# Performance work log

Measured on AMD Instinct MI355X. Metric: run time of the kernel, lower is better.

## Reference

```python
import math
import jax, jax.numpy as jnp
import numpy as np

D_MODEL = 1024
N_HEADS = 16
D_K = D_MODEL // N_HEADS


def _alibi_slopes(n_heads):
    # Faithful to the torch _get_slopes: slopes[i] = 2**(-8 + i), subsampled if
    # n_heads is not a power of two.
    power = 2 ** math.ceil(math.log2(n_heads))
    slopes = np.array([2.0 ** (-8 + i) for i in range(power)], dtype=np.float32)
    if n_heads != power:
        ratio = power // n_heads
        slopes = slopes[np.arange(0, power, ratio)][:n_heads]
    return jnp.asarray(slopes)


def setup_inputs() -> dict:
    key = jax.random.key(0)
    ks = jax.random.split(key, 11)
    B, S, D = 2, 2048, D_MODEL
    w = 0.02  # weight init scale
    return {
        "query": jax.random.normal(ks[0], (B, S, D), jnp.float32),
        "key": jax.random.normal(ks[1], (B, S, D), jnp.float32),
        "value": jax.random.normal(ks[2], (B, S, D), jnp.float32),
        "Wq": jax.random.normal(ks[3], (D, D), jnp.float32) * w,
        "bq": jax.random.normal(ks[4], (D,), jnp.float32) * w,
        "Wk": jax.random.normal(ks[5], (D, D), jnp.float32) * w,
        "bk": jax.random.normal(ks[6], (D,), jnp.float32) * w,
        "Wv": jax.random.normal(ks[7], (D, D), jnp.float32) * w,
        "bv": jax.random.normal(ks[8], (D,), jnp.float32) * w,
        "Wo": jax.random.normal(ks[9], (D, D), jnp.float32) * w,
        "bo": jax.random.normal(ks[10], (D,), jnp.float32) * w,
    }


def reference(query, key, value, Wq, bq, Wk, bk, Wv, bv, Wo, bo):
    B, Sq, D = query.shape
    Sk = key.shape[1]
    H, dk = N_HEADS, D_K

    # projections (torch Linear: x @ W.T + b)
    q = (query @ Wq.T + bq).reshape(B, Sq, H, dk).transpose(0, 2, 1, 3)  # [B,H,Sq,dk]
    k = (key @ Wk.T + bk).reshape(B, Sk, H, dk).transpose(0, 2, 1, 3)    # [B,H,Sk,dk]
    v = (value @ Wv.T + bv).reshape(B, Sk, H, dk).transpose(0, 2, 1, 3)  # [B,H,Sk,dk]

    scores = jnp.einsum("bhqd,bhkd->bhqk", q, k) / jnp.sqrt(jnp.float32(dk))

    # ALiBi bias: slopes[h] * (i - j), non-causal path (is_causal=False)
    dist = (jnp.arange(Sq)[:, None] - jnp.arange(Sk)[None, :]).astype(scores.dtype)
    slopes = _alibi_slopes(H)
    scores = scores + slopes[None, :, None, None] * dist[None, None, :, :]

    attn = jax.nn.softmax(scores, axis=-1)
    out = jnp.einsum("bhqk,bhkd->bhqd", attn, v)          # [B,H,Sq,dk]
    out = out.transpose(0, 2, 1, 3).reshape(B, Sq, D)     # [B,Sq,D]
    return out @ Wo.T + bo
```

## Files before the change

kernel.cpp:

```cpp
#include <hip/hip_runtime.h>

typedef __bf16 bf16_t;
typedef bf16_t bf16x8 __attribute__((ext_vector_type(8)));
typedef float f32x4 __attribute__((ext_vector_type(4)));
typedef float f32x16 __attribute__((ext_vector_type(16)));
typedef unsigned short u16x4 __attribute__((ext_vector_type(4)));
typedef unsigned int u32x4v __attribute__((ext_vector_type(4)));
typedef unsigned int u32;

#define DEV static __device__ __forceinline__


DEV unsigned short f2bf(float f) {
  unsigned int u = __builtin_bit_cast(unsigned int, f);
  u = (u + 0x7fffu + ((u >> 16) & 1u)) >> 16;
  return (unsigned short)u;
}

DEV float fexp2(float x) {
  float r;
  asm("v_exp_f32 %0, %1" : "=v"(r) : "v"(x));
  return r;
}

DEV u32 cvtpk(float lo, float hi_) {
  u32 r;
  asm("v_cvt_pk_bf16_f32 %0, %1, %2" : "=v"(r) : "v"(lo), "v"(hi_));
  return r;
}

DEV void plswap(u32& a, u32& b) {
  asm("v_permlane32_swap_b32 %0, %1" : "+v"(a), "+v"(b));
}

DEV void async_ld16(const unsigned short* gsrc, unsigned short* lbase, int lane) {
#if __has_builtin(__builtin_amdgcn_global_load_lds)
  __builtin_amdgcn_global_load_lds(
      (const __attribute__((address_space(1))) unsigned int*)(const void*)gsrc,
      (__attribute__((address_space(3))) unsigned int*)(void*)lbase, 16, 0, 0);
#else
  *reinterpret_cast<u32x4v*>(reinterpret_cast<char*>(lbase) + lane * 16) =
      *reinterpret_cast<const u32x4v*>(gsrc);
#endif
}


DEV void cvt_body(const float* __restrict__ src, unsigned short* __restrict__ dst, int i) {
  const float4* s = reinterpret_cast<const float4*>(src) + (size_t)i * 2;
  float4 a = s[0], c = s[1];
  u16x4 lo = {f2bf(a.x), f2bf(a.y), f2bf(a.z), f2bf(a.w)};
  u16x4 hi = {f2bf(c.x), f2bf(c.y), f2bf(c.z), f2bf(c.w)};
  u16x4* d = reinterpret_cast<u16x4*>(dst) + (size_t)i * 2;
  d[0] = lo;
  d[1] = hi;
}

__global__ __launch_bounds__(256) void cvt_all(
    const float* __restrict__ q, const float* __restrict__ k, const float* __restrict__ v,
    const float* __restrict__ Wq, const float* __restrict__ Wk, const float* __restrict__ Wv,
    const float* __restrict__ Wo, unsigned short* dq, unsigned short* dk, unsigned short* dv,
    unsigned short* dWq, unsigned short* dWk, unsigned short* dWv, unsigned short* dWo) {
  const int bid = blockIdx.x;
  const float* src;
  unsigned short* dst;
  int i;
  if (bid < 6144) {
    const int z = bid >> 11;
    src = z == 0 ? q : z == 1 ? k : v;
    dst = z == 0 ? dq : z == 1 ? dk : dv;
    i = (bid & 2047) * 256 + threadIdx.x;
  } else {
    const int z = (bid - 6144) >> 9;
    src = z == 0 ? Wq : z == 1 ? Wk : z == 2 ? Wv : Wo;
    dst = z == 0 ? dWq : z == 1 ? dWk : z == 2 ? dWv : dWo;
    i = ((bid - 6144) & 511) * 256 + threadIdx.x;
  }
  cvt_body(src, dst, i);
}


DEV void stage_b128(const unsigned short* __restrict__ G, int row0, int k0,
                    unsigned short* lbuf, int lane, int wv) {
#pragma unroll
  for (int r = 0; r < 4; ++r) {
    const int rowB = (r * 4 + wv) * 8 + (lane >> 3);
    const int chunk = (lane & 7) ^ (rowB & 7);
    async_ld16(G + (size_t)(row0 + rowB) * 1024 + k0 + chunk * 8, lbuf + (r * 4 + wv) * 512,
               lane);
  }
}

DEV void mfma_step(const unsigned short* lA, const unsigned short* lB, int lane, int wm, int wn,
                   f32x4 acc[4][4]) {
#pragma unroll
  for (int kk = 0; kk < 2; ++kk) {
    bf16x8 af[4], bfr[4];
#pragma unroll
    for (int f = 0; f < 4; ++f) {
      const int rowA = wm * 64 + f * 16 + (lane & 15);
      const int cA = (kk * 4 + (lane >> 4)) ^ (rowA & 7);
      af[f] = *reinterpret_cast<const bf16x8*>(lA + rowA * 64 + cA * 8);
      const int rowB = wn * 64 + f * 16 + (lane & 15);
      const int cB = (kk * 4 + (lane >> 4)) ^ (rowB & 7);
      bfr[f] = *reinterpret_cast<const bf16x8*>(lB + rowB * 64 + cB * 8);
    }
#pragma unroll
    for (int i = 0; i < 4; ++i)
#pragma unroll
      for (int j = 0; j < 4; ++j)
        acc[i][j] = __builtin_amdgcn_mfma_f32_16x16x32_bf16(af[i], bfr[j], acc[i][j], 0, 0, 0);
  }
}

DEV void gemm_core(const unsigned short* __restrict__ X, const unsigned short* __restrict__ W,
                   unsigned short* lA0, unsigned short* lA1, unsigned short* lB0,
                   unsigned short* lB1, int bm0, int bn0, int lane, int wv, int wm, int wn,
                   f32x4 acc[4][4]) {
  stage_b128(X, bm0, 0, lA0, lane, wv);
  stage_b128(W, bn0, 0, lB0, lane, wv);
  __syncthreads();
  for (int kt = 0; kt < 16; ++kt) {
    unsigned short* lA = (kt & 1) ? lA1 : lA0;
    unsigned short* lB = (kt & 1) ? lB1 : lB0;
    unsigned short* nA = (kt & 1) ? lA0 : lA1;
    unsigned short* nB = (kt & 1) ? lB0 : lB1;
    if (kt < 15) {
      stage_b128(X, bm0, (kt + 1) * 64, nA, lane, wv);
      stage_b128(W, bn0, (kt + 1) * 64, nB, lane, wv);
    }
    mfma_step(lA, lB, lane, wm, wn, acc);
    __syncthreads();
  }
}


__global__ __launch_bounds__(256) void gemm_qkv_kernel(
    const unsigned short* __restrict__ Xq, const unsigned short* __restrict__ Xk,
    const unsigned short* __restrict__ Xv, const unsigned short* __restrict__ Wq,
    const unsigned short* __restrict__ Wk, const unsigned short* __restrict__ Wv,
    const float* __restrict__ bq, const float* __restrict__ bk, const float* __restrict__ bv,
    unsigned short* __restrict__ Qp, unsigned short* __restrict__ Kp,
    unsigned short* __restrict__ Vp, unsigned* __restrict__ nb2) {
  __shared__ unsigned short lA[2][8192];
  __shared__ unsigned short lB[2][8192];
  const unsigned short* X;
  const unsigned short* W;
  const float* bias;
  unsigned short* dst;
  if (blockIdx.z == 0) { X = Xq; W = Wq; bias = bq; dst = Qp; }
  else if (blockIdx.z == 1) { X = Xk; W = Wk; bias = bk; dst = Kp; }
  else { X = Xv; W = Wv; bias = bv; dst = Vp; }
  const bool zV = (blockIdx.z == 2);
  const bool zK = (blockIdx.z == 1) && (nb2 != nullptr);
  const int lane = threadIdx.x & 63, wv = threadIdx.x >> 6;
  const int wm = wv >> 1, wn = wv & 1;
  const int bm0 = blockIdx.x * 128, bn0 = blockIdx.y * 128;
  f32x4 acc[4][4] = {};
  gemm_core(X, W, lA[0], lA[1], lB[0], lB[1], bm0, bn0, lane, wv, wm, wn, acc);
  float rowmax = 0.0f;
#pragma unroll
  for (int i = 0; i < 4; ++i) {
    const int mbase = bm0 + wm * 64 + i * 16 + ((lane >> 4) << 2);
#pragma unroll
    for (int r = 0; r < 4; ++r) {
      const int m = mbase + r;
      const int b = m >> 11, s = m & 2047;
      float ssp = 0.0f;
#pragma unroll
      for (int j = 0; j < 4; ++j) {
        const int n = bn0 + wn * 64 + j * 16 + (lane & 15);
        const float val = acc[i][j][r] + bias[n];
        const unsigned short v16 = f2bf(val);
        const int h = n >> 6, d = n & 63;
        if (zV)
          dst[((size_t)(b * 16 + h) * 64 + d) * 2048 + s] = v16;
        else
          dst[((size_t)(b * 16 + h) * 2048 + s) * 64 + d] = v16;
        ssp = __builtin_fmaf(val, val, ssp);
      }
      if (zK) {
        ssp += __shfl_xor(ssp, 1);
        ssp += __shfl_xor(ssp, 2);
        ssp += __shfl_xor(ssp, 4);
        ssp += __shfl_xor(ssp, 8);
        rowmax = fmaxf(rowmax, ssp);
      }
    }
  }
  if (zK) {
    rowmax = fmaxf(rowmax, __shfl_xor(rowmax, 16));
    rowmax = fmaxf(rowmax, __shfl_xor(rowmax, 32));
    if (lane == 0) {
      const int bh = (bm0 >> 11) * 16 + blockIdx.y * 2 + wn;
      atomicMax(nb2 + bh, __float_as_uint(rowmax));
    }
  }
}


__global__ __launch_bounds__(256) void gemm_out_kernel(const unsigned short* __restrict__ X,
                                                       const unsigned short* __restrict__ W,
                                                       const float* __restrict__ bias,
                                                       float* __restrict__ out) {
  __shared__ unsigned short lA[2][8192];
  __shared__ unsigned short lB[2][8192];
  const int lane = threadIdx.x & 63, wv = threadIdx.x >> 6;
  const int wm = wv >> 1, wn = wv & 1;
  const int bm0 = blockIdx.x * 128, bn0 = blockIdx.y * 128;
  f32x4 acc[4][4] = {};
  gemm_core(X, W, lA[0], lA[1], lB[0], lB[1], bm0, bn0, lane, wv, wm, wn, acc);
#pragma unroll
  for (int i = 0; i < 4; ++i) {
    const int mbase = bm0 + wm * 64 + i * 16 + ((lane >> 4) << 2);
#pragma unroll
    for (int j = 0; j < 4; ++j) {
      const int n = bn0 + wn * 64 + j * 16 + (lane & 15);
      const float bia = bias[n];
#pragma unroll
      for (int r = 0; r < 4; ++r) out[(size_t)(mbase + r) * 1024 + n] = acc[i][j][r] + bia;
    }
  }
}


__global__ __launch_bounds__(256) void knorm_kernel(const unsigned short* __restrict__ Kp,
                                                    unsigned* __restrict__ nb2) {
  const int bh = blockIdx.y;
  const int s = blockIdx.x * 256 + threadIdx.x;
  const u32x4v* row = reinterpret_cast<const u32x4v*>(Kp + ((size_t)bh * 2048 + s) * 64);
  float ss = 0.0f;
#pragma unroll
  for (int c = 0; c < 8; ++c) {
    u32x4v u = row[c];
#pragma unroll
    for (int e = 0; e < 4; ++e) {
      const float lo = __builtin_bit_cast(float, u[e] << 16);
      const float hi = __builtin_bit_cast(float, u[e] & 0xFFFF0000u);
      ss = __builtin_fmaf(lo, lo, ss);
      ss = __builtin_fmaf(hi, hi, ss);
    }
  }
#pragma unroll
  for (int off = 1; off <= 32; off <<= 1) ss = fmaxf(ss, __shfl_xor(ss, off));
  if ((threadIdx.x & 63) == 0) atomicMax(nb2 + bh, __float_as_uint(ss));
}


__global__ __launch_bounds__(128) void attn_prepass(const unsigned short* __restrict__ Qp,
                                                    const unsigned short* __restrict__ Kp,
                                                    const unsigned* __restrict__ nb2,
                                                    float* __restrict__ mfA,
                                                    float* __restrict__ bltA) {
  __shared__ float sred[4];
  const int lane = threadIdx.x & 63, wv = threadIdx.x >> 6;
  const int lq = lane & 31, hi = lane >> 5;
  const int qt = blockIdx.x, bh = blockIdx.y, h = bh & 15;
  const float L2E = 1.4426950408889634f;
  const float slope2 = ldexpf(L2E, h - 8);
  const float SC2 = 0.125f * L2E;
  const size_t headoff = (size_t)bh * 2048 * 64;
  const unsigned short* Qh = Qp + headoff;
  const unsigned short* Kh = Kp + headoff;
  const int q_glob = qt * 64 + wv * 32 + lq;

  bf16x8 qf[4];
#pragma unroll
  for (int tt = 0; tt < 4; ++tt)
    qf[tt] = *reinterpret_cast<const bf16x8*>(Qh + (size_t)q_glob * 64 + tt * 16 + hi * 8);

  float qq = 0.0f;
#pragma unroll
  for (int tt = 0; tt < 4; ++tt)
#pragma unroll
    for (int e = 0; e < 8; ++e) {
      const float x = (float)qf[tt][e];
      qq = __builtin_fmaf(x, x, qq);
    }
  qq += __shfl_xor(qq, 32);
#pragma unroll
  for (int off = 1; off <= 16; off <<= 1) qq = fmaxf(qq, __shfl_xor(qq, off));

  f32x16 s0 = {}, s1 = {};
#pragma unroll
  for (int tt = 0; tt < 4; ++tt) {
    bf16x8 k0 = *reinterpret_cast<const bf16x8*>(Kh + (size_t)lq * 64 + tt * 16 + hi * 8);
    s0 = __builtin_amdgcn_mfma_f32_32x32x16_bf16(k0, qf[tt], s0, 0, 0, 0);
    bf16x8 k1 = *reinterpret_cast<const bf16x8*>(Kh + (size_t)(32 + lq) * 64 + tt * 16 + hi * 8);
    s1 = __builtin_amdgcn_mfma_f32_32x32x16_bf16(k1, qf[tt], s1, 0, 0, 0);
  }
  float zmax = -3.0e38f;
#pragma unroll
  for (int r = 0; r < 16; ++r) {
    const float cb = -slope2 * (float)(4 * hi + (r & 3) + 8 * (r >> 2));
    const float x0 = __builtin_fmaf(s0[r], SC2, cb);
    const float x1 = __builtin_fmaf(s1[r], SC2, cb - slope2 * 32.0f);
    zmax = fmaxf(zmax, fmaxf(x0, x1));
  }
  zmax = fmaxf(zmax, __shfl_xor(zmax, 32));
  float zmin = zmax;
#pragma unroll
  for (int off = 1; off <= 16; off <<= 1) zmin = fminf(zmin, __shfl_xor(zmin, off));
  if (lane == 0) {
    sred[wv] = zmin;
    sred[2 + wv] = qq;
  }
  __syncthreads();
  if (threadIdx.x == 0) {
    const float mf = fminf(sred[0], sred[1]);
    const float qn = sqrtf(fmaxf(sred[2], sred[3]));
    const float nk = sqrtf(__uint_as_float(nb2[bh]));
    mfA[bh * 32 + qt] = mf;
    bltA[bh * 32 + qt] = qn * nk * SC2;
  }
}


DEV void stage_tile64(const unsigned short* __restrict__ Gbase, size_t stride, int colbase,
                      unsigned short* lbuf, int lane, int wv) {
#pragma unroll
  for (int i = 0; i < 4; ++i) {
    const int r = i * 16 + wv * 8 + (lane >> 3);
    const int chunk = (lane & 7) ^ (r & 7);
    async_ld16(Gbase + (size_t)r * stride + colbase + chunk * 8, lbuf + (i * 16 + wv * 8) * 64,
               lane);
  }
}

__global__ __launch_bounds__(128) void attn_split_kernel(
    const unsigned short* __restrict__ Qp, const unsigned short* __restrict__ Kp,
    const unsigned short* __restrict__ VTp, const float* __restrict__ mfA,
    const float* __restrict__ bltA, float* __restrict__ ML, float* __restrict__ Opart, int Ct,
    int nsplit) {
  __shared__ unsigned short Kb[2][64 * 64];
  __shared__ unsigned short Vb[2][64 * 64];
  const int lane = threadIdx.x & 63, wv = threadIdx.x >> 6;
  const int lq = lane & 31, hi = lane >> 5;
  const int qt = blockIdx.x, sp = blockIdx.y, bh = blockIdx.z;
  const int h = bh & 15;
  const int idx = bh * 32 + qt;
  const float L2E = 1.4426950408889634f;
  const float slope2 = ldexpf(L2E, h - 8);
  const float SC2 = 0.125f * L2E;
  const float m_floor = mfA[idx], blt = bltA[idx];
  const float tf = (blt - m_floor + 34.0f) / (slope2 * 64.0f);
  const int T_act = min(32, (int)tf + 1);
  const int t0 = sp * Ct;
  const int nt = min(Ct, T_act - t0);
  float* mlb = ML + ((size_t)idx * nsplit + sp) * 128;
  if (nt <= 0) {
    mlb[threadIdx.x] = threadIdx.x < 64 ? -3.0e38f : 0.0f;
    return;
  }
  float* ob = Opart + ((size_t)idx * nsplit + sp) * 4096;
  const size_t headoff = (size_t)bh * 2048 * 64;
  const unsigned short* Qh = Qp + headoff;
  const unsigned short* Kh = Kp + headoff;
  const unsigned short* VTh = VTp + headoff;
  const int q_glob = qt * 64 + wv * 32 + lq;

  float cb0[16], cb1[16];
#pragma unroll
  for (int r = 0; r < 16; ++r) {
    cb0[r] = -slope2 * (float)(4 * hi + (r & 3) + 8 * (r >> 2));
    cb1[r] = cb0[r] - slope2 * 32.0f;
  }

  bf16x8 qf[4];
#pragma unroll
  for (int tt = 0; tt < 4; ++tt)
    qf[tt] = *reinterpret_cast<const bf16x8*>(Qh + (size_t)q_glob * 64 + tt * 16 + hi * 8);

  stage_tile64(Kh + (size_t)(t0 * 64) * 64, 64, 0, Kb[0], lane, wv);
  stage_tile64(VTh, 2048, t0 * 64, Vb[0], lane, wv);
  __syncthreads();

  f32x16 acc0 = {}, acc1 = {};
  float m_run = m_floor, l_run = 0.0f;

  for (int ti = 0; ti < nt; ++ti) {
    const int kv0 = (t0 + ti) * 64;
    const float s2k = slope2 * (float)kv0;
    const unsigned short* Kc = Kb[ti & 1];
    const unsigned short* Vc = Vb[ti & 1];
    if (ti + 1 < nt) {
      stage_tile64(Kh + (size_t)(kv0 + 64) * 64, 64, 0, Kb[(ti + 1) & 1], lane, wv);
      stage_tile64(VTh, 2048, kv0 + 64, Vb[(ti + 1) & 1], lane, wv);
    }
    f32x16 s0 = {}, s1 = {};
    __builtin_amdgcn_s_setprio(1);
#pragma unroll
    for (int tt = 0; tt < 4; ++tt) {
      {
        const int row = lq;
        const int ch = (tt * 2 + hi) ^ (row & 7);
        bf16x8 kf = *reinterpret_cast<const bf16x8*>(Kc + row * 64 + ch * 8);
        s0 = __builtin_amdgcn_mfma_f32_32x32x16_bf16(kf, qf[tt], s0, 0, 0, 0);
      }
      {
        const int row = 32 + lq;
        const int ch = (tt * 2 + hi) ^ (row & 7);
        bf16x8 kf = *reinterpret_cast<const bf16x8*>(Kc + row * 64 + ch * 8);
        s1 = __builtin_amdgcn_mfma_f32_32x32x16_bf16(kf, qf[tt], s1, 0, 0, 0);
      }
    }
    __builtin_amdgcn_s_setprio(0);
    float zmax = -3.0e38f;
#pragma unroll
    for (int r = 0; r < 16; ++r) {
      s0[r] = __builtin_fmaf(s0[r], SC2, cb0[r]);
      s1[r] = __builtin_fmaf(s1[r], SC2, cb1[r]);
      zmax = fmaxf(zmax, fmaxf(s0[r], s1[r]));
    }
    zmax = fmaxf(zmax, __shfl_xor(zmax, 32));
    const float tmax_true = zmax - s2k;
    if (__any(tmax_true > m_run + 8.0f)) {
      const float m_new = fmaxf(m_run, tmax_true);
      const float alpha = fexp2(m_run - m_new);
      m_run = m_new;
      l_run *= alpha;
      acc0 *= alpha;
      acc1 *= alpha;
    }
    const float mm = m_run + s2k;
    float ps0 = 0.0f, ps1 = 0.0f;
#pragma unroll
    for (int r = 0; r < 16; ++r) {
      const float p0 = fexp2(s0[r] - mm);
      const float p1 = fexp2(s1[r] - mm);
      s0[r] = p0;
      s1[r] = p1;
      ps0 += p0;
      ps1 += p1;
    }
    float psum = ps0 + ps1;
    psum += __shfl_xor(psum, 32);
    l_run += psum;
    bf16x8 pf[4];
#pragma unroll
    for (int half = 0; half < 2; ++half) {
      u32 w0 = cvtpk(s0[half * 8 + 0], s0[half * 8 + 1]);
      u32 w2 = cvtpk(s0[half * 8 + 4], s0[half * 8 + 5]);
      plswap(w0, w2);
      u32 w1 = cvtpk(s0[half * 8 + 2], s0[half * 8 + 3]);
      u32 w3 = cvtpk(s0[half * 8 + 6], s0[half * 8 + 7]);
      plswap(w1, w3);
      u32x4v ww = {w0, w1, w2, w3};
      pf[half] = __builtin_bit_cast(bf16x8, ww);
    }
#pragma unroll
    for (int half = 0; half < 2; ++half) {
      u32 w0 = cvtpk(s1[half * 8 + 0], s1[half * 8 + 1]);
      u32 w2 = cvtpk(s1[half * 8 + 4], s1[half * 8 + 5]);
      plswap(w0, w2);
      u32 w1 = cvtpk(s1[half * 8 + 2], s1[half * 8 + 3]);
      u32 w3 = cvtpk(s1[half * 8 + 6], s1[half * 8 + 7]);
      plswap(w1, w3);
      u32x4v ww = {w0, w1, w2, w3};
      pf[2 + half] = __builtin_bit_cast(bf16x8, ww);
    }
    __builtin_amdgcn_s_setprio(1);
#pragma unroll
    for (int tt = 0; tt < 4; ++tt) {
      {
        const int row = lq;
        const int ch = (tt * 2 + hi) ^ (row & 7);
        bf16x8 vf = *reinterpret_cast<const bf16x8*>(Vc + row * 64 + ch * 8);
        acc0 = __builtin_amdgcn_mfma_f32_32x32x16_bf16(vf, pf[tt], acc0, 0, 0, 0);
      }
      {
        const int row = 32 + lq;
        const int ch = (tt * 2 + hi) ^ (row & 7);
        bf16x8 vf = *reinterpret_cast<const bf16x8*>(Vc + row * 64 + ch * 8);
        acc1 = __builtin_amdgcn_mfma_f32_32x32x16_bf16(vf, pf[tt], acc1, 0, 0, 0);
      }
    }
    __builtin_amdgcn_s_setprio(0);
    __syncthreads();
  }
  const int qloc = wv * 32 + lq;
  if (hi == 0) {
    mlb[qloc] = m_run;
    mlb[64 + qloc] = l_run;
  }
#pragma unroll
  for (int g = 0; g < 4; ++g) {
    f32x4 w0, w1;
#pragma unroll
    for (int e = 0; e < 4; ++e) {
      w0[e] = acc0[g * 4 + e];
      w1[e] = acc1[g * 4 + e];
    }
    *reinterpret_cast<f32x4*>(ob + qloc * 64 + g * 8 + 4 * hi) = w0;
    *reinterpret_cast<f32x4*>(ob + qloc * 64 + 32 + g * 8 + 4 * hi) = w1;
  }
}


__global__ __launch_bounds__(256) void attn_combine(const float* __restrict__ ML,
                                                    const float* __restrict__ Opart,
                                                    unsigned short* __restrict__ Ob, int nsplit) {
  const int idx = blockIdx.x;
  const int bh = idx >> 5, qt = idx & 31;
  const int h = bh & 15, b = bh >> 4;
  const int q = threadIdx.x >> 2, d0 = (threadIdx.x & 3) * 16;
  const float* mlb = ML + (size_t)idx * nsplit * 128;
  const float* ob = Opart + (size_t)idx * nsplit * 4096;
  float m_g = -3.0e38f;
  for (int s = 0; s < nsplit; ++s) m_g = fmaxf(m_g, mlb[s * 128 + q]);
  float l = 0.0f;
  f32x4 acc[4] = {};
  for (int s = 0; s < nsplit; ++s) {
    const float ms = mlb[s * 128 + q], ls = mlb[s * 128 + 64 + q];
    const float w = fexp2(ms - m_g);
    const float wl = w * ls;
    if (wl > 0.0f) {
      l += wl;
      const f32x4* src = reinterpret_cast<const f32x4*>(ob + (size_t)s * 4096 + q * 64 + d0);
#pragma unroll
      for (int j = 0; j < 4; ++j) {
        f32x4 v = src[j];
#pragma unroll
        for (int e = 0; e < 4; ++e) acc[j][e] = __builtin_fmaf(w, v[e], acc[j][e]);
      }
    }
  }
  const float invl = 1.0f / l;
  unsigned short* orow = Ob + ((size_t)(b * 2048 + qt * 64 + q)) * 1024 + h * 64 + d0;
#pragma unroll
  for (int j = 0; j < 4; ++j) {
    u16x4 pk;
#pragma unroll
    for (int e = 0; e < 4; ++e) pk[e] = f2bf(acc[j][e] * invl);
    *reinterpret_cast<u16x4*>(orow + j * 4) = pk;
  }
}


extern "C" void kernel_launch(void* const* d_in, const int* in_sizes, int n_in, void* d_out,
                              int out_size, void* d_ws, size_t ws_size, hipStream_t stream) {
  const float* q = (const float*)d_in[0];
  const float* k = (const float*)d_in[1];
  const float* v = (const float*)d_in[2];
  const float* Wq = (const float*)d_in[3];
  const float* bq = (const float*)d_in[4];
  const float* Wk = (const float*)d_in[5];
  const float* bk = (const float*)d_in[6];
  const float* Wv = (const float*)d_in[7];
  const float* bv = (const float*)d_in[8];
  const float* Wo = (const float*)d_in[9];
  const float* bo = (const float*)d_in[10];

  char* ws = (char*)d_ws;
  const size_t MB = 1024 * 1024;
  unsigned short* qb = (unsigned short*)(ws + 0 * MB);
  unsigned short* kb = (unsigned short*)(ws + 8 * MB);
  unsigned short* vb = (unsigned short*)(ws + 16 * MB);
  unsigned short* Wqb = (unsigned short*)(ws + 24 * MB);
  unsigned short* Wkb = (unsigned short*)(ws + 26 * MB);
  unsigned short* Wvb = (unsigned short*)(ws + 28 * MB);
  unsigned short* Wob = (unsigned short*)(ws + 30 * MB);
  unsigned short* Qp = (unsigned short*)(ws + 32 * MB);
  unsigned short* Kp = (unsigned short*)(ws + 40 * MB);
  unsigned short* VTp = (unsigned short*)(ws + 48 * MB);
  unsigned short* Obf = (unsigned short*)(ws + 0 * MB);

  int nsplit;
  float *mfA, *bltA, *ML, *Opart;
  unsigned* nb2;
  bool fold_knorm;
  if (ws_size >= (size_t)121 * MB) nsplit = 4;
  else if (ws_size >= (size_t)89 * MB) nsplit = 2;
  else nsplit = 1;
  if (ws_size >= (size_t)73 * MB) {
    fold_knorm = true;
    nb2 = (unsigned*)(ws + 56 * MB);
    mfA = (float*)(ws + 24 * MB + 4096);
    bltA = (float*)(ws + 24 * MB + 8192);
    ML = (float*)(ws + 26 * MB + 65536);
    Opart = (float*)(ws + 56 * MB + 4096);
  } else {
    fold_knorm = false;
    nsplit = 1;
    nb2 = (unsigned*)(ws + 26 * MB);
    mfA = (float*)(ws + 26 * MB + 4096);
    bltA = (float*)(ws + 26 * MB + 8192);
    ML = (float*)(ws + 26 * MB + 65536);
    Opart = (float*)(ws + 8 * MB);
  }
  const int Ct = 32 / nsplit;

  cvt_all<<<8192, 256, 0, stream>>>(q, k, v, Wq, Wk, Wv, Wo, qb, kb, vb, Wqb, Wkb, Wvb, Wob);
  hipMemsetAsync(nb2, 0, 64 * sizeof(unsigned), stream);
  gemm_qkv_kernel<<<dim3(32, 8, 3), 256, 0, stream>>>(qb, kb, vb, Wqb, Wkb, Wvb, bq, bk, bv, Qp,
                                                      Kp, VTp, fold_knorm ? nb2 : nullptr);
  if (!fold_knorm) knorm_kernel<<<dim3(8, 32), 256, 0, stream>>>(Kp, nb2);
  attn_prepass<<<dim3(32, 32), 128, 0, stream>>>(Qp, Kp, nb2, mfA, bltA);
  attn_split_kernel<<<dim3(32, nsplit, 32), 128, 0, stream>>>(Qp, Kp, VTp, mfA, bltA, ML, Opart,
                                                              Ct, nsplit);
  attn_combine<<<1024, 256, 0, stream>>>(ML, Opart, Obf, nsplit);
  gemm_out_kernel<<<dim3(32, 8), 256, 0, stream>>>(Obf, Wob, bo, (float*)d_out);
}
```

Measured before the change: 124.6 us.

## Fuse attention prepass into split kernel and fold nb2 zeroing into convert

Removes the separate attn_prepass launch. Each attn_split block now computes its own query-norm and first-tile score minimum, from which it derives the skip bound. The nb2 memset is moved into the cvt_all kernel when fold_knorm holds, and the GEMM staging precomputes per-row global pointers and fully unrolls the k-loop. This saves two launches and a round-trip through mfA/bltA, but every split block (nsplit of them per q-tile) redoes the prepass work, and the unrolled loop adds code size and register pressure.

```diff
diff --git a/kernel.cpp b/kernel.cpp
--- a/kernel.cpp
+++ b/kernel.cpp
@@ -59,8 +59,10 @@
     const float* __restrict__ q, const float* __restrict__ k, const float* __restrict__ v,
     const float* __restrict__ Wq, const float* __restrict__ Wk, const float* __restrict__ Wv,
     const float* __restrict__ Wo, unsigned short* dq, unsigned short* dk, unsigned short* dv,
-    unsigned short* dWq, unsigned short* dWk, unsigned short* dWv, unsigned short* dWo) {
+    unsigned short* dWq, unsigned short* dWk, unsigned short* dWv, unsigned short* dWo,
+    unsigned* __restrict__ nb2z) {
   const int bid = blockIdx.x;
+  if (nb2z != nullptr && bid == 0 && threadIdx.x < 64) nb2z[threadIdx.x] = 0u;
   const float* src;
   unsigned short* dst;
   int i;
@@ -79,17 +81,6 @@
 }
 
 
-DEV void stage_b128(const unsigned short* __restrict__ G, int row0, int k0,
-                    unsigned short* lbuf, int lane, int wv) {
-#pragma unroll
-  for (int r = 0; r < 4; ++r) {
-    const int rowB = (r * 4 + wv) * 8 + (lane >> 3);
-    const int chunk = (lane & 7) ^ (rowB & 7);
-    async_ld16(G + (size_t)(row0 + rowB) * 1024 + k0 + chunk * 8, lbuf + (r * 4 + wv) * 512,
-               lane);
-  }
-}
-
 DEV void mfma_step(const unsigned short* lA, const unsigned short* lB, int lane, int wm, int wn,
                    f32x4 acc[4][4]) {
 #pragma unroll
@@ -116,17 +107,33 @@
                    unsigned short* lA0, unsigned short* lA1, unsigned short* lB0,
                    unsigned short* lB1, int bm0, int bn0, int lane, int wv, int wm, int wn,
                    f32x4 acc[4][4]) {
-  stage_b128(X, bm0, 0, lA0, lane, wv);
-  stage_b128(W, bn0, 0, lB0, lane, wv);
+  const unsigned short* pa[4];
+  const unsigned short* pb[4];
+#pragma unroll
+  for (int r = 0; r < 4; ++r) {
+    const int row = (r * 4 + wv) * 8 + (lane >> 3);
+    const int chunk = (lane & 7) ^ (row & 7);
+    pa[r] = X + (size_t)(bm0 + row) * 1024 + chunk * 8;
+    pb[r] = W + (size_t)(bn0 + row) * 1024 + chunk * 8;
+  }
+#pragma unroll
+  for (int r = 0; r < 4; ++r) {
+    async_ld16(pa[r], lA0 + (r * 4 + wv) * 512, lane);
+    async_ld16(pb[r], lB0 + (r * 4 + wv) * 512, lane);
+  }
   __syncthreads();
+#pragma unroll
   for (int kt = 0; kt < 16; ++kt) {
-    unsigned short* lA = (kt & 1) ? lA1 : lA0;
-    unsigned short* lB = (kt & 1) ? lB1 : lB0;
+    const unsigned short* lA = (kt & 1) ? lA1 : lA0;
+    const unsigned short* lB = (kt & 1) ? lB1 : lB0;
     unsigned short* nA = (kt & 1) ? lA0 : lA1;
     unsigned short* nB = (kt & 1) ? lB0 : lB1;
     if (kt < 15) {
-      stage_b128(X, bm0, (kt + 1) * 64, nA, lane, wv);
-      stage_b128(W, bn0, (kt + 1) * 64, nB, lane, wv);
+#pragma unroll
+      for (int r = 0; r < 4; ++r) {
+        async_ld16(pa[r] + (kt + 1) * 64, nA + (r * 4 + wv) * 512, lane);
+        async_ld16(pb[r] + (kt + 1) * 64, nB + (r * 4 + wv) * 512, lane);
+      }
     }
     mfma_step(lA, lB, lane, wm, wn, acc);
     __syncthreads();
@@ -246,75 +253,6 @@
 }
 
 
-__global__ __launch_bounds__(128) void attn_prepass(const unsigned short* __restrict__ Qp,
-                                                    const unsigned short* __restrict__ Kp,
-                                                    const unsigned* __restrict__ nb2,
-                                                    float* __restrict__ mfA,
-                                                    float* __restrict__ bltA) {
-  __shared__ float sred[4];
-  const int lane = threadIdx.x & 63, wv = threadIdx.x >> 6;
-  const int lq = lane & 31, hi = lane >> 5;
-  const int qt = blockIdx.x, bh = blockIdx.y, h = bh & 15;
-  const float L2E = 1.4426950408889634f;
-  const float slope2 = ldexpf(L2E, h - 8);
-  const float SC2 = 0.125f * L2E;
-  const size_t headoff = (size_t)bh * 2048 * 64;
-  const unsigned short* Qh = Qp + headoff;
-  const unsigned short* Kh = Kp + headoff;
-  const int q_glob = qt * 64 + wv * 32 + lq;
-
-  bf16x8 qf[4];
-#pragma unroll
-  for (int tt = 0; tt < 4; ++tt)
-    qf[tt] = *reinterpret_cast<const bf16x8*>(Qh + (size_t)q_glob * 64 + tt * 16 + hi * 8);
-
-  float qq = 0.0f;
-#pragma unroll
-  for (int tt = 0; tt < 4; ++tt)
-#pragma unroll
-    for (int e = 0; e < 8; ++e) {
-      const float x = (float)qf[tt][e];
-      qq = __builtin_fmaf(x, x, qq);
-    }
-  qq += __shfl_xor(qq, 32);
-#pragma unroll
-  for (int off = 1; off <= 16; off <<= 1) qq = fmaxf(qq, __shfl_xor(qq, off));
-
-  f32x16 s0 = {}, s1 = {};
-#pragma unroll
-  for (int tt = 0; tt < 4; ++tt) {
-    bf16x8 k0 = *reinterpret_cast<const bf16x8*>(Kh + (size_t)lq * 64 + tt * 16 + hi * 8);
-    s0 = __builtin_amdgcn_mfma_f32_32x32x16_bf16(k0, qf[tt], s0, 0, 0, 0);
-    bf16x8 k1 = *reinterpret_cast<const bf16x8*>(Kh + (size_t)(32 + lq) * 64 + tt * 16 + hi * 8);
-    s1 = __builtin_amdgcn_mfma_f32_32x32x16_bf16(k1, qf[tt], s1, 0, 0, 0);
-  }
-  float zmax = -3.0e38f;
-#pragma unroll
-  for (int r = 0; r < 16; ++r) {
-    const float cb = -slope2 * (float)(4 * hi + (r & 3) + 8 * (r >> 2));
-    const float x0 = __builtin_fmaf(s0[r], SC2, cb);
-    const float x1 = __builtin_fmaf(s1[r], SC2, cb - slope2 * 32.0f);
-    zmax = fmaxf(zmax, fmaxf(x0, x1));
-  }
-  zmax = fmaxf(zmax, __shfl_xor(zmax, 32));
-  float zmin = zmax;
-#pragma unroll
-  for (int off = 1; off <= 16; off <<= 1) zmin = fminf(zmin, __shfl_xor(zmin, off));
-  if (lane == 0) {
-    sred[wv] = zmin;
-    sred[2 + wv] = qq;
-  }
-  __syncthreads();
-  if (threadIdx.x == 0) {
-    const float mf = fminf(sred[0], sred[1]);
-    const float qn = sqrtf(fmaxf(sred[2], sred[3]));
-    const float nk = sqrtf(__uint_as_float(nb2[bh]));
-    mfA[bh * 32 + qt] = mf;
-    bltA[bh * 32 + qt] = qn * nk * SC2;
-  }
-}
-
-
 DEV void stage_tile64(const unsigned short* __restrict__ Gbase, size_t stride, int colbase,
                       unsigned short* lbuf, int lane, int wv) {
 #pragma unroll
@@ -328,11 +266,11 @@
 
 __global__ __launch_bounds__(128) void attn_split_kernel(
     const unsigned short* __restrict__ Qp, const unsigned short* __restrict__ Kp,
-    const unsigned short* __restrict__ VTp, const float* __restrict__ mfA,
-    const float* __restrict__ bltA, float* __restrict__ ML, float* __restrict__ Opart, int Ct,
-    int nsplit) {
+    const unsigned short* __restrict__ VTp, const unsigned* __restrict__ nb2,
+    float* __restrict__ ML, float* __restrict__ Opart, int Ct, int nsplit) {
   __shared__ unsigned short Kb[2][64 * 64];
   __shared__ unsigned short Vb[2][64 * 64];
+  __shared__ float sred[4];
   const int lane = threadIdx.x & 63, wv = threadIdx.x >> 6;
   const int lq = lane & 31, hi = lane >> 5;
   const int qt = blockIdx.x, sp = blockIdx.y, bh = blockIdx.z;
@@ -341,17 +279,8 @@
   const float L2E = 1.4426950408889634f;
   const float slope2 = ldexpf(L2E, h - 8);
   const float SC2 = 0.125f * L2E;
-  const float m_floor = mfA[idx], blt = bltA[idx];
-  const float tf = (blt - m_floor + 34.0f) / (slope2 * 64.0f);
-  const int T_act = min(32, (int)tf + 1);
   const int t0 = sp * Ct;
-  const int nt = min(Ct, T_act - t0);
   float* mlb = ML + ((size_t)idx * nsplit + sp) * 128;
-  if (nt <= 0) {
-    mlb[threadIdx.x] = threadIdx.x < 64 ? -3.0e38f : 0.0f;
-    return;
-  }
-  float* ob = Opart + ((size_t)idx * nsplit + sp) * 4096;
   const size_t headoff = (size_t)bh * 2048 * 64;
   const unsigned short* Qh = Qp + headoff;
   const unsigned short* Kh = Kp + headoff;
@@ -372,7 +301,56 @@
 
   stage_tile64(Kh + (size_t)(t0 * 64) * 64, 64, 0, Kb[0], lane, wv);
   stage_tile64(VTh, 2048, t0 * 64, Vb[0], lane, wv);
+
+  float qq = 0.0f;
+#pragma unroll
+  for (int tt = 0; tt < 4; ++tt)
+#pragma unroll
+    for (int e = 0; e < 8; ++e) {
+      const float x = (float)qf[tt][e];
+      qq = __builtin_fmaf(x, x, qq);
+    }
+  qq += __shfl_xor(qq, 32);
+#pragma unroll
+  for (int off = 1; off <= 16; off <<= 1) qq = fmaxf(qq, __shfl_xor(qq, off));
+  {
+    f32x16 s0 = {}, s1 = {};
+#pragma unroll
+    for (int tt = 0; tt < 4; ++tt) {
+      bf16x8 k0 = *reinterpret_cast<const bf16x8*>(Kh + (size_t)lq * 64 + tt * 16 + hi * 8);
+      s0 = __builtin_amdgcn_mfma_f32_32x32x16_bf16(k0, qf[tt], s0, 0, 0, 0);
+      bf16x8 k1 =
+          *reinterpret_cast<const bf16x8*>(Kh + (size_t)(32 + lq) * 64 + tt * 16 + hi * 8);
+      s1 = __builtin_amdgcn_mfma_f32_32x32x16_bf16(k1, qf[tt], s1, 0, 0, 0);
+    }
+    float zmax = -3.0e38f;
+#pragma unroll
+    for (int r = 0; r < 16; ++r) {
+      const float x0 = __builtin_fmaf(s0[r], SC2, cb0[r]);
+      const float x1 = __builtin_fmaf(s1[r], SC2, cb1[r]);
+      zmax = fmaxf(zmax, fmaxf(x0, x1));
+    }
+    zmax = fmaxf(zmax, __shfl_xor(zmax, 32));
+    float zmin = zmax;
+#pragma unroll
+    for (int off = 1; off <= 16; off <<= 1) zmin = fminf(zmin, __shfl_xor(zmin, off));
+    if (lane == 0) {
+      sred[wv] = zmin;
+      sred[2 + wv] = qq;
+    }
+  }
   __syncthreads();
+  const float m_floor = fminf(sred[0], sred[1]);
+  const float qn = sqrtf(fmaxf(sred[2], sred[3]));
+  const float blt = qn * sqrtf(__uint_as_float(nb2[bh])) * SC2;
+  const float tf = (blt - m_floor + 34.0f) / (slope2 * 64.0f);
+  const int T_act = min(32, (int)tf + 1);
+  const int nt = min(Ct, T_act - t0);
+  if (nt <= 0) {
+    mlb[threadIdx.x] = threadIdx.x < 64 ? -3.0e38f : 0.0f;
+    return;
+  }
+  float* ob = Opart + ((size_t)idx * nsplit + sp) * 4096;
 
   f32x16 acc0 = {}, acc1 = {};
   float m_run = m_floor, l_run = 0.0f;
@@ -565,7 +543,7 @@
   unsigned short* Obf = (unsigned short*)(ws + 0 * MB);
 
   int nsplit;
-  float *mfA, *bltA, *ML, *Opart;
+  float *ML, *Opart;
   unsigned* nb2;
   bool fold_knorm;
   if (ws_size >= (size_t)121 * MB) nsplit = 4;
@@ -574,29 +552,27 @@
   if (ws_size >= (size_t)73 * MB) {
     fold_knorm = true;
     nb2 = (unsigned*)(ws + 56 * MB);
-    mfA = (float*)(ws + 24 * MB + 4096);
-    bltA = (float*)(ws + 24 * MB + 8192);
     ML = (float*)(ws + 26 * MB + 65536);
     Opart = (float*)(ws + 56 * MB + 4096);
   } else {
     fold_knorm = false;
     nsplit = 1;
     nb2 = (unsigned*)(ws + 26 * MB);
-    mfA = (float*)(ws + 26 * MB + 4096);
-    bltA = (float*)(ws + 26 * MB + 8192);
     ML = (float*)(ws + 26 * MB + 65536);
     Opart = (float*)(ws + 8 * MB);
   }
   const int Ct = 32 / nsplit;
 
-  cvt_all<<<8192, 256, 0, stream>>>(q, k, v, Wq, Wk, Wv, Wo, qb, kb, vb, Wqb, Wkb, Wvb, Wob);
-  hipMemsetAsync(nb2, 0, 64 * sizeof(unsigned), stream);
+  cvt_all<<<8192, 256, 0, stream>>>(q, k, v, Wq, Wk, Wv, Wo, qb, kb, vb, Wqb, Wkb, Wvb, Wob,
+                                    fold_knorm ? nb2 : nullptr);
   gemm_qkv_kernel<<<dim3(32, 8, 3), 256, 0, stream>>>(qb, kb, vb, Wqb, Wkb, Wvb, bq, bk, bv, Qp,
                                                       Kp, VTp, fold_knorm ? nb2 : nullptr);
-  if (!fold_knorm) knorm_kernel<<<dim3(8, 32), 256, 0, stream>>>(Kp, nb2);
-  attn_prepass<<<dim3(32, 32), 128, 0, stream>>>(Qp, Kp, nb2, mfA, bltA);
-  attn_split_kernel<<<dim3(32, nsplit, 32), 128, 0, stream>>>(Qp, Kp, VTp, mfA, bltA, ML, Opart,
-                                                              Ct, nsplit);
+  if (!fold_knorm) {
+    hipMemsetAsync(nb2, 0, 64 * sizeof(unsigned), stream);
+    knorm_kernel<<<dim3(8, 32), 256, 0, stream>>>(Kp, nb2);
+  }
+  attn_split_kernel<<<dim3(32, nsplit, 32), 128, 0, stream>>>(Qp, Kp, VTp, nb2, ML, Opart, Ct,
+                                                              nsplit);
   attn_combine<<<1024, 256, 0, stream>>>(ML, Opart, Obf, nsplit);
   gemm_out_kernel<<<dim3(32, 8), 256, 0, stream>>>(Obf, Wob, bo, (float*)d_out);
 }
```

Result: no change. 124.4 us (-0.2%).
